# Performance work log

Measured on AMD Instinct MI355X. Metric: run time of the kernel, lower is better.

The kernel has to match this reference:

```python
import jax, jax.numpy as jnp
import numpy as np

D_MODEL = 1024
N_HEAD = 16
D_HEAD = D_MODEL // N_HEAD
D_FF = 4096
EPS = 1e-5


def _layernorm(x, gamma, beta):
    mu = jnp.mean(x, axis=-1, keepdims=True)
    var = jnp.mean(jnp.square(x - mu), axis=-1, keepdims=True)
    return (x - mu) * jax.lax.rsqrt(var + EPS) * gamma + beta


def setup_inputs() -> dict:
    key = jax.random.key(0)
    ks = jax.random.split(key, 16)
    s = 1.0 / np.sqrt(D_MODEL)
    sf = 1.0 / np.sqrt(D_FF)
    return {
        "src": jax.random.normal(ks[0], (8, 1024, D_MODEL), dtype=jnp.float32),
        "Wq": jax.random.uniform(ks[1], (D_MODEL, D_MODEL), jnp.float32, -s, s),
        "bq": jnp.zeros((D_MODEL,), jnp.float32),
        "Wk": jax.random.uniform(ks[2], (D_MODEL, D_MODEL), jnp.float32, -s, s),
        "bk": jnp.zeros((D_MODEL,), jnp.float32),
        "Wv": jax.random.uniform(ks[3], (D_MODEL, D_MODEL), jnp.float32, -s, s),
        "bv": jnp.zeros((D_MODEL,), jnp.float32),
        "Wo": jax.random.uniform(ks[4], (D_MODEL, D_MODEL), jnp.float32, -s, s),
        "bo": jnp.zeros((D_MODEL,), jnp.float32),
        "W1": jax.random.uniform(ks[5], (D_MODEL, D_FF), jnp.float32, -s, s),
        "b1": jnp.zeros((D_FF,), jnp.float32),
        "W2": jax.random.uniform(ks[6], (D_FF, D_MODEL), jnp.float32, -sf, sf),
        "b2": jnp.zeros((D_MODEL,), jnp.float32),
        "g1": jnp.ones((D_MODEL,), jnp.float32),
        "beta1": jnp.zeros((D_MODEL,), jnp.float32),
        "g2": jnp.ones((D_MODEL,), jnp.float32),
        "beta2": jnp.zeros((D_MODEL,), jnp.float32),
    }


def reference(src, Wq, bq, Wk, bk, Wv, bv, Wo, bo, W1, b1, W2, b2, g1, beta1, g2, beta2):
    B, S, _ = src.shape
    x = _layernorm(src, g1, beta1)
    # QKV projections -> [B, H, S, Dh]
    def split_heads(t):
        return t.reshape(B, S, N_HEAD, D_HEAD).transpose(0, 2, 1, 3)
    q = split_heads(x @ Wq + bq)
    k = split_heads(x @ Wk + bk)
    v = split_heads(x @ Wv + bv)
    # SymbolicAttention (canonical graph): softmax(q k^T / sqrt(d_head)) v
    scores = jnp.einsum('bhqd,bhkd->bhqk', q, k) / np.sqrt(D_HEAD).astype(np.float32)
    attn = jax.nn.softmax(scores, axis=-1)
    ctx = jnp.einsum('bhqk,bhkd->bhqd', attn, v)
    ctx = ctx.transpose(0, 2, 1, 3).reshape(B, S, D_MODEL)
    src = src + (ctx @ Wo + bo)  # dropout is identity in eval
    y = _layernorm(src, g2, beta2)
    ffn = jax.nn.relu(y @ W1 + b1) @ W2 + b2
    return src + ffn
```

## Files before the change

### kernel.cpp

```cpp
#include <hip/hip_runtime.h>
#include <stdint.h>

#define D_MODEL 1024
#define N_HEAD  16
#define D_HEAD  64
#define D_FF    4096
#define SEQ     1024
#define BATCH   8
#define M_TOK   (BATCH*SEQ)

typedef __attribute__((ext_vector_type(8))) short bf16x8;
typedef __attribute__((ext_vector_type(4))) float f32x4;

__device__ __forceinline__ float bf2f(unsigned short u) {
    union { unsigned int u; float f; } x; x.u = ((unsigned int)u) << 16; return x.f;
}
__device__ __forceinline__ unsigned short f2bf(float f) {
    union { float f; unsigned int u; } x; x.f = f;
    unsigned int r = x.u + 0x7fffu + ((x.u >> 16) & 1u);
    return (unsigned short)(r >> 16);
}

typedef const __attribute__((address_space(1))) unsigned int* gas_t;
typedef __attribute__((address_space(3))) unsigned int* las_t;
__device__ __forceinline__ void gl_lds16(const unsigned short* g, unsigned short* l) {
    __builtin_amdgcn_global_load_lds((gas_t)g, (las_t)l, 16, 0, 0);
}

__global__ __launch_bounds__(256) void transpose_cvt(
        const float* __restrict__ src, unsigned short* __restrict__ dst,
        int R, int C)
{
    __shared__ float t[32][33];
    const int tx = threadIdx.x & 31, ty = threadIdx.x >> 5;
    const int c0 = blockIdx.x * 32, r0 = blockIdx.y * 32;
    #pragma unroll
    for (int i = 0; i < 32; i += 8)
        t[ty + i][tx] = src[(size_t)(r0 + ty + i) * C + c0 + tx];
    __syncthreads();
    #pragma unroll
    for (int i = 0; i < 32; i += 8)
        dst[(size_t)(c0 + ty + i) * R + r0 + tx] = f2bf(t[tx][ty + i]);
}

__global__ __launch_bounds__(256) void ln_kernel(
        const float* __restrict__ x, const float* __restrict__ g,
        const float* __restrict__ be, unsigned short* __restrict__ out)
{
    const int row = blockIdx.x, tid = threadIdx.x;
    const f32x4 v = *(const f32x4*)(x + (size_t)row * D_MODEL + tid * 4);
    float s  = v[0] + v[1] + v[2] + v[3];
    float ss = v[0]*v[0] + v[1]*v[1] + v[2]*v[2] + v[3]*v[3];
    #pragma unroll
    for (int o = 1; o < 64; o <<= 1) { s += __shfl_xor(s, o); ss += __shfl_xor(ss, o); }
    __shared__ float sa[4], sb[4];
    const int wv = tid >> 6;
    if ((tid & 63) == 0) { sa[wv] = s; sb[wv] = ss; }
    __syncthreads();
    s  = sa[0] + sa[1] + sa[2] + sa[3];
    ss = sb[0] + sb[1] + sb[2] + sb[3];
    const float mu   = s * (1.0f / D_MODEL);
    const float rstd = rsqrtf(ss * (1.0f / D_MODEL) - mu * mu + 1e-5f);
    const f32x4 gv = *(const f32x4*)(g  + tid * 4);
    const f32x4 bv = *(const f32x4*)(be + tid * 4);
    unsigned short w[4];
    #pragma unroll
    for (int j = 0; j < 4; j++) w[j] = f2bf((v[j] - mu) * rstd * gv[j] + bv[j]);
    *(uint2*)(out + (size_t)row * D_MODEL + tid * 4) = *(uint2*)w;
}

template<int MODE>
__global__ __launch_bounds__(256) void gemm_bf16_tn(
        const unsigned short* __restrict__ A,
        const unsigned short* __restrict__ BT,
        const float* __restrict__ bias,
        const float* __restrict__ bias2,
        const float* __restrict__ bias3,
        const float* __restrict__ resid,
        void* __restrict__ Cout,
        int M, int N, int K)
{
    constexpr bool SWAP = (MODE != 3);
    __shared__ unsigned short As[128 * 64];
    __shared__ unsigned short Bs[128 * 64];

    const int tid  = threadIdx.x;
    const int wave = tid >> 6, lane = tid & 63;
    const int quad = lane >> 4, l16 = lane & 15;

    int m0, n0;
    if (MODE == 2) {
        const int G = gridDim.x;
        const int f = blockIdx.x + G * blockIdx.y;
        m0 = ((f & 7) + 8 * ((f >> 3) / G)) * 128;
        n0 = ((f >> 3) % G) * 128;
    } else {
        m0 = blockIdx.y * 128;
        n0 = blockIdx.x * 128;
    }
    const int wm = (wave >> 1) * 64, wn = (wave & 1) * 64;

    const int st_row = wave * 8 + ((tid >> 3) & 7);
    const int st_g   = (tid & 7) ^ ((tid >> 3) & 7);
    const unsigned short* gA = A  + (size_t)(m0 + st_row) * K + st_g * 8;
    const unsigned short* gB = BT + (size_t)(n0 + st_row) * K + st_g * 8;
    unsigned short* lA = As + wave * 512;
    unsigned short* lB = Bs + wave * 512;
    const int rx = l16 & 7;

    f32x4 acc[4][4] = {};

    for (int k0 = 0; k0 < K; k0 += 64) {
        __syncthreads();
        #pragma unroll
        for (int j = 0; j < 4; j++) {
            gl_lds16(gA + (size_t)j * 32 * K + k0, lA + j * 2048);
            gl_lds16(gB + (size_t)j * 32 * K + k0, lB + j * 2048);
        }
        __syncthreads();

        #pragma unroll
        for (int h = 0; h < 2; h++) {
            bf16x8 af[4], bfr[4];
            #pragma unroll
            for (int mi = 0; mi < 4; mi++)
                af[mi] = *(const bf16x8*)(As + (wm + mi * 16 + l16) * 64
                                          + ((h * 4 + quad) ^ rx) * 8);
            #pragma unroll
            for (int ni = 0; ni < 4; ni++)
                bfr[ni] = *(const bf16x8*)(Bs + (wn + ni * 16 + l16) * 64
                                           + ((h * 4 + quad) ^ rx) * 8);
            #pragma unroll
            for (int mi = 0; mi < 4; mi++)
                #pragma unroll
                for (int ni = 0; ni < 4; ni++)
                    acc[mi][ni] = SWAP
                        ? __builtin_amdgcn_mfma_f32_16x16x32_bf16(
                              bfr[ni], af[mi], acc[mi][ni], 0, 0, 0)
                        : __builtin_amdgcn_mfma_f32_16x16x32_bf16(
                              af[mi], bfr[ni], acc[mi][ni], 0, 0, 0);
        }
    }

    if (SWAP) {
        #pragma unroll
        for (int mi = 0; mi < 4; mi++) {
            const int row = m0 + wm + mi * 16 + l16;
            #pragma unroll
            for (int ni = 0; ni < 4; ni++) {
                const int col = n0 + wn + ni * 16 + quad * 4;
                const f32x4 bs4 = *(const f32x4*)(bias + col);
                if (MODE == 1) {
                    unsigned short w[4];
                    #pragma unroll
                    for (int r = 0; r < 4; r++)
                        w[r] = f2bf(fmaxf(acc[mi][ni][r] + bs4[r], 0.0f));
                    *(uint2*)((unsigned short*)Cout + (size_t)row * N + col)
                        = *(uint2*)w;
                } else {
                    const f32x4 rv = *(const f32x4*)(resid + (size_t)row * N + col);
                    f32x4 o;
                    #pragma unroll
                    for (int r = 0; r < 4; r++)
                        o[r] = acc[mi][ni][r] + bs4[r] + rv[r];
                    *(f32x4*)((float*)Cout + (size_t)row * N + col) = o;
                }
            }
        }
    } else {
        #pragma unroll
        for (int mi = 0; mi < 4; mi++) {
            const int row_b = m0 + wm + mi * 16 + quad * 4;
            #pragma unroll
            for (int ni = 0; ni < 4; ni++) {
                const int col = n0 + wn + ni * 16 + l16;
                if (col < 2048) {
                    const float sc  = (col < 1024) ? 0.125f : 1.0f;
                    const float bsv = (col < 1024) ? bias[col] : bias2[col - 1024];
                    unsigned short* dst = (unsigned short*)Cout
                        + (size_t)(col >> 10) * M_TOK * 1024;
                    #pragma unroll
                    for (int r = 0; r < 4; r++)
                        dst[(size_t)(row_b + r) * 1024 + (col & 1023)] =
                            f2bf((acc[mi][ni][r] + bsv) * sc);
                } else {
                    const int cc = col - 2048;
                    const float bsv = bias3[cc];
                    const int bb = row_b >> 10, s = row_b & 1023;
                    const int h = cc >> 6, dd = cc & 63;
                    unsigned short w[4];
                    #pragma unroll
                    for (int r = 0; r < 4; r++)
                        w[r] = f2bf(acc[mi][ni][r] + bsv);
                    *(uint2*)((unsigned short*)Cout + (size_t)2 * M_TOK * 1024
                              + ((size_t)((bb * 16 + h) * 64 + dd)) * 1024 + s)
                        = *(uint2*)w;
                }
            }
        }
    }
}

#define ASTR 72
__global__ __launch_bounds__(256) void attn_mfma(
        const unsigned short* __restrict__ Q,
        const unsigned short* __restrict__ K,
        const unsigned short* __restrict__ VT,
        unsigned short* __restrict__ CTX)
{
    __shared__ unsigned short Ks[64 * ASTR];
    __shared__ unsigned short Vs[64 * ASTR];
    __shared__ unsigned short Ps[128 * ASTR];

    const int tid  = threadIdx.x;
    const int wave = tid >> 6, lane = tid & 63;
    const int quad = lane >> 4, l16 = lane & 15;
    const int bh = blockIdx.y;
    const int q0 = blockIdx.x * 128;
    const size_t baseQ = (size_t)(bh >> 4) * SEQ * D_MODEL + (size_t)(bh & 15) * D_HEAD;
    const size_t baseV = (size_t)bh * D_HEAD * SEQ;
    const int strip = wave * 32;

    bf16x8 qf[2][2];
    #pragma unroll
    for (int mt = 0; mt < 2; mt++)
        #pragma unroll
        for (int h = 0; h < 2; h++)
            qf[mt][h] = *(const bf16x8*)(Q + baseQ
                        + (size_t)(q0 + strip + mt * 16 + l16) * D_MODEL
                        + h * 32 + quad * 8);

    f32x4 of[2][4] = {};
    float l_p[2][4] = {};

    for (int c = 0; c < SEQ / 64; c++) {
        const int k0 = c * 64;
        __syncthreads();
        #pragma unroll
        for (int u = tid; u < 512; u += 256) {
            const int r = u >> 3, g = (u & 7) * 8;
            *(uint4*)(Ks + r * ASTR + g) =
                *(const uint4*)(K + baseQ + (size_t)(k0 + r) * D_MODEL + g);
            *(uint4*)(Vs + r * ASTR + g) =
                *(const uint4*)(VT + baseV + (size_t)r * SEQ + k0 + g);
        }
        __syncthreads();

        bf16x8 kf[4][2];
        #pragma unroll
        for (int kt = 0; kt < 4; kt++)
            #pragma unroll
            for (int h = 0; h < 2; h++)
                kf[kt][h] = *(const bf16x8*)(Ks + (kt * 16 + l16) * ASTR + h * 32 + quad * 8);

        #pragma unroll
        for (int mt = 0; mt < 2; mt++) {
            f32x4 s[4] = {};
            #pragma unroll
            for (int h = 0; h < 2; h++)
                #pragma unroll
                for (int kt = 0; kt < 4; kt++)
                    s[kt] = __builtin_amdgcn_mfma_f32_16x16x32_bf16(
                            qf[mt][h], kf[kt][h], s[kt], 0, 0, 0);
            #pragma unroll
            for (int kt = 0; kt < 4; kt++)
                #pragma unroll
                for (int r = 0; r < 4; r++) {
                    const float p = __expf(s[kt][r]);
                    l_p[mt][r] += p;
                    Ps[(strip + mt * 16 + quad * 4 + r) * ASTR + kt * 16 + l16] = f2bf(p);
                }
        }

        bf16x8 pf[2][2];
        #pragma unroll
        for (int mt = 0; mt < 2; mt++)
            #pragma unroll
            for (int h = 0; h < 2; h++)
                pf[mt][h] = *(const bf16x8*)(Ps + (strip + mt * 16 + l16) * ASTR
                                             + h * 32 + quad * 8);
        #pragma unroll
        for (int nt = 0; nt < 4; nt++) {
            bf16x8 vf[2];
            #pragma unroll
            for (int h = 0; h < 2; h++)
                vf[h] = *(const bf16x8*)(Vs + (nt * 16 + l16) * ASTR + h * 32 + quad * 8);
            #pragma unroll
            for (int mt = 0; mt < 2; mt++)
                #pragma unroll
                for (int h = 0; h < 2; h++)
                    of[mt][nt] = __builtin_amdgcn_mfma_f32_16x16x32_bf16(
                            pf[mt][h], vf[h], of[mt][nt], 0, 0, 0);
        }
    }

    #pragma unroll
    for (int mt = 0; mt < 2; mt++) {
        float inv[4];
        #pragma unroll
        for (int r = 0; r < 4; r++) {
            float l = l_p[mt][r];
            #pragma unroll
            for (int o = 1; o < 16; o <<= 1) l += __shfl_xor(l, o);
            inv[r] = 1.0f / l;
        }
        #pragma unroll
        for (int nt = 0; nt < 4; nt++)
            #pragma unroll
            for (int r = 0; r < 4; r++)
                CTX[baseQ + (size_t)(q0 + strip + mt * 16 + quad * 4 + r) * D_MODEL
                    + nt * 16 + l16] = f2bf(of[mt][nt][r] * inv[r]);
    }
}

extern "C" void kernel_launch(void* const* d_in, const int* in_sizes, int n_in,
                              void* d_out, int out_size, void* d_ws, size_t ws_size,
                              hipStream_t stream)
{
    (void)in_sizes; (void)n_in; (void)out_size; (void)ws_size;
    const float* src = (const float*)d_in[0];
    const float* Wq  = (const float*)d_in[1];
    const float* bq  = (const float*)d_in[2];
    const float* Wk  = (const float*)d_in[3];
    const float* bk  = (const float*)d_in[4];
    const float* Wv  = (const float*)d_in[5];
    const float* bv  = (const float*)d_in[6];
    const float* Wo  = (const float*)d_in[7];
    const float* bo  = (const float*)d_in[8];
    const float* W1  = (const float*)d_in[9];
    const float* b1  = (const float*)d_in[10];
    const float* W2  = (const float*)d_in[11];
    const float* b2  = (const float*)d_in[12];
    const float* g1  = (const float*)d_in[13];
    const float* be1 = (const float*)d_in[14];
    const float* g2  = (const float*)d_in[15];
    const float* be2 = (const float*)d_in[16];
    float* out = (float*)d_out;

    unsigned short* wqkvT = (unsigned short*)d_ws;
    unsigned short* woT = wqkvT + (size_t)3 * 1024 * 1024;
    unsigned short* w1T = woT + 1024 * 1024;
    unsigned short* w2T = w1T + (size_t)4096 * 1024;
    unsigned short* xn  = w2T + (size_t)1024 * 4096;
    unsigned short* q   = xn  + (size_t)M_TOK * D_MODEL;
    unsigned short* k   = q   + (size_t)M_TOK * D_MODEL;
    unsigned short* vT  = k   + (size_t)M_TOK * D_MODEL;
    unsigned short* ctx = vT  + (size_t)M_TOK * D_MODEL;
    unsigned short* hid = ctx + (size_t)M_TOK * D_MODEL;

    const dim3 blk(256);

    transpose_cvt<<<dim3(32, 32),  blk, 0, stream>>>(Wq, wqkvT,                 1024, 1024);
    transpose_cvt<<<dim3(32, 32),  blk, 0, stream>>>(Wk, wqkvT + 1024 * 1024,   1024, 1024);
    transpose_cvt<<<dim3(32, 32),  blk, 0, stream>>>(Wv, wqkvT + 2 * 1024 * 1024, 1024, 1024);
    transpose_cvt<<<dim3(32, 32),  blk, 0, stream>>>(Wo, woT, 1024, 1024);
    transpose_cvt<<<dim3(128, 32), blk, 0, stream>>>(W1, w1T, 1024, 4096);
    transpose_cvt<<<dim3(32, 128), blk, 0, stream>>>(W2, w2T, 4096, 1024);

    ln_kernel<<<M_TOK, blk, 0, stream>>>(src, g1, be1, xn);

    gemm_bf16_tn<3><<<dim3(24, 64), blk, 0, stream>>>(
        xn, wqkvT, bq, bk, bv, nullptr, q, M_TOK, 3072, D_MODEL);

    attn_mfma<<<dim3(SEQ / 128, BATCH * N_HEAD), blk, 0, stream>>>(q, k, vT, ctx);

    gemm_bf16_tn<2><<<dim3(8, 64), blk, 0, stream>>>(
        ctx, woT, bo, nullptr, nullptr, src, out, M_TOK, D_MODEL, D_MODEL);

    ln_kernel<<<M_TOK, blk, 0, stream>>>(out, g2, be2, xn);

    gemm_bf16_tn<1><<<dim3(32, 64), blk, 0, stream>>>(
        xn, w1T, b1, nullptr, nullptr, nullptr, hid, M_TOK, D_FF, D_MODEL);

    gemm_bf16_tn<2><<<dim3(8, 64), blk, 0, stream>>>(
        hid, w2T, b2, nullptr, nullptr, out, out, M_TOK, D_MODEL, D_FF);
}
```

Before: 501.0 us.

## Switch GEMMs to 32x32x16 MFMA and split QKV projection into QK and V launches

All GEMM variants now use 32x32x16 bf16 MFMA with 2x2 accumulator tiles per wave instead of 16x16x32 with 4x4 tiles. This halves the LDS fragment loads per MFMA and gives wider contiguous epilogue writes. The fused QKV projection is split in two: Q/K go through a row-major mode with vectorized stores, and V goes through a separate transposed-store launch. That removes the per-element strided scalar stores for Q and K, at the cost of one extra kernel launch.

After: 536.8 us. 7.2% more time.

```diff
diff --git a/kernel.cpp b/kernel.cpp
--- a/kernel.cpp
+++ b/kernel.cpp
@@ -9,8 +9,9 @@
 #define BATCH   8
 #define M_TOK   (BATCH*SEQ)
 
-typedef __attribute__((ext_vector_type(8))) short bf16x8;
-typedef __attribute__((ext_vector_type(4))) float f32x4;
+typedef __attribute__((ext_vector_type(8)))  short bf16x8;
+typedef __attribute__((ext_vector_type(4)))  float f32x4;
+typedef __attribute__((ext_vector_type(16))) float f32x16;
 
 __device__ __forceinline__ float bf2f(unsigned short u) {
     union { unsigned int u; float f; } x; x.u = ((unsigned int)u) << 16; return x.f;
@@ -75,7 +76,6 @@
         const unsigned short* __restrict__ BT,
         const float* __restrict__ bias,
         const float* __restrict__ bias2,
-        const float* __restrict__ bias3,
         const float* __restrict__ resid,
         void* __restrict__ Cout,
         int M, int N, int K)
@@ -86,7 +86,7 @@
 
     const int tid  = threadIdx.x;
     const int wave = tid >> 6, lane = tid & 63;
-    const int quad = lane >> 4, l16 = lane & 15;
+    const int l32 = lane & 31, khalf = lane >> 5;
 
     int m0, n0;
     if (MODE == 2) {
@@ -106,9 +106,9 @@
     const unsigned short* gB = BT + (size_t)(n0 + st_row) * K + st_g * 8;
     unsigned short* lA = As + wave * 512;
     unsigned short* lB = Bs + wave * 512;
-    const int rx = l16 & 7;
-
-    f32x4 acc[4][4] = {};
+    const int rx = l32 & 7;
+
+    f32x16 acc[2][2] = {};
 
     for (int k0 = 0; k0 < K; k0 += 64) {
         __syncthreads();
@@ -120,79 +120,84 @@
         __syncthreads();
 
         #pragma unroll
-        for (int h = 0; h < 2; h++) {
-            bf16x8 af[4], bfr[4];
-            #pragma unroll
-            for (int mi = 0; mi < 4; mi++)
-                af[mi] = *(const bf16x8*)(As + (wm + mi * 16 + l16) * 64
-                                          + ((h * 4 + quad) ^ rx) * 8);
-            #pragma unroll
-            for (int ni = 0; ni < 4; ni++)
-                bfr[ni] = *(const bf16x8*)(Bs + (wn + ni * 16 + l16) * 64
-                                           + ((h * 4 + quad) ^ rx) * 8);
-            #pragma unroll
-            for (int mi = 0; mi < 4; mi++)
-                #pragma unroll
-                for (int ni = 0; ni < 4; ni++)
+        for (int s = 0; s < 4; s++) {
+            const int slot = ((s * 2 + khalf) ^ rx) * 8;
+            bf16x8 af[2], bfr[2];
+            #pragma unroll
+            for (int mi = 0; mi < 2; mi++)
+                af[mi] = *(const bf16x8*)(As + (wm + mi * 32 + l32) * 64 + slot);
+            #pragma unroll
+            for (int ni = 0; ni < 2; ni++)
+                bfr[ni] = *(const bf16x8*)(Bs + (wn + ni * 32 + l32) * 64 + slot);
+            #pragma unroll
+            for (int mi = 0; mi < 2; mi++)
+                #pragma unroll
+                for (int ni = 0; ni < 2; ni++)
                     acc[mi][ni] = SWAP
-                        ? __builtin_amdgcn_mfma_f32_16x16x32_bf16(
+                        ? __builtin_amdgcn_mfma_f32_32x32x16_bf16(
                               bfr[ni], af[mi], acc[mi][ni], 0, 0, 0)
-                        : __builtin_amdgcn_mfma_f32_16x16x32_bf16(
+                        : __builtin_amdgcn_mfma_f32_32x32x16_bf16(
                               af[mi], bfr[ni], acc[mi][ni], 0, 0, 0);
         }
     }
 
     if (SWAP) {
         #pragma unroll
-        for (int mi = 0; mi < 4; mi++) {
-            const int row = m0 + wm + mi * 16 + l16;
-            #pragma unroll
-            for (int ni = 0; ni < 4; ni++) {
-                const int col = n0 + wn + ni * 16 + quad * 4;
-                const f32x4 bs4 = *(const f32x4*)(bias + col);
-                if (MODE == 1) {
+        for (int mi = 0; mi < 2; mi++) {
+            const int row = m0 + wm + mi * 32 + l32;
+            #pragma unroll
+            for (int ni = 0; ni < 2; ni++) {
+                #pragma unroll
+                for (int g = 0; g < 4; g++) {
+                    const int col = n0 + wn + ni * 32 + 8 * g + 4 * khalf;
+                    if (MODE == 1) {
+                        const f32x4 b4 = *(const f32x4*)(bias + col);
+                        unsigned short w[4];
+                        #pragma unroll
+                        for (int r = 0; r < 4; r++)
+                            w[r] = f2bf(fmaxf(acc[mi][ni][4 * g + r] + b4[r], 0.0f));
+                        *(uint2*)((unsigned short*)Cout + (size_t)row * N + col)
+                            = *(uint2*)w;
+                    } else if (MODE == 2) {
+                        const f32x4 b4 = *(const f32x4*)(bias + col);
+                        const f32x4 rv = *(const f32x4*)(resid + (size_t)row * N + col);
+                        f32x4 o;
+                        #pragma unroll
+                        for (int r = 0; r < 4; r++)
+                            o[r] = acc[mi][ni][4 * g + r] + b4[r] + rv[r];
+                        *(f32x4*)((float*)Cout + (size_t)row * N + col) = o;
+                    } else {
+                        const float sc = (col < 1024) ? 0.125f : 1.0f;
+                        const f32x4 b4 = *(const f32x4*)(
+                            ((col < 1024) ? bias : bias2) + (col & 1023));
+                        unsigned short w[4];
+                        #pragma unroll
+                        for (int r = 0; r < 4; r++)
+                            w[r] = f2bf((acc[mi][ni][4 * g + r] + b4[r]) * sc);
+                        *(uint2*)((unsigned short*)Cout
+                                  + (size_t)(col >> 10) * M_TOK * 1024
+                                  + (size_t)row * 1024 + (col & 1023)) = *(uint2*)w;
+                    }
+                }
+            }
+        }
+    } else {
+        #pragma unroll
+        for (int mi = 0; mi < 2; mi++) {
+            #pragma unroll
+            for (int ni = 0; ni < 2; ni++) {
+                const int col = n0 + wn + ni * 32 + l32;
+                const float bsv = bias[col];
+                const int h = col >> 6, dd = col & 63;
+                #pragma unroll
+                for (int g = 0; g < 4; g++) {
+                    const int rowb = m0 + wm + mi * 32 + 8 * g + 4 * khalf;
+                    const int bb = rowb >> 10, s = rowb & 1023;
                     unsigned short w[4];
                     #pragma unroll
                     for (int r = 0; r < 4; r++)
-                        w[r] = f2bf(fmaxf(acc[mi][ni][r] + bs4[r], 0.0f));
-                    *(uint2*)((unsigned short*)Cout + (size_t)row * N + col)
-                        = *(uint2*)w;
-                } else {
-                    const f32x4 rv = *(const f32x4*)(resid + (size_t)row * N + col);
-                    f32x4 o;
-                    #pragma unroll
-                    for (int r = 0; r < 4; r++)
-                        o[r] = acc[mi][ni][r] + bs4[r] + rv[r];
-                    *(f32x4*)((float*)Cout + (size_t)row * N + col) = o;
-                }
-            }
-        }
-    } else {
-        #pragma unroll
-        for (int mi = 0; mi < 4; mi++) {
-            const int row_b = m0 + wm + mi * 16 + quad * 4;
-            #pragma unroll
-            for (int ni = 0; ni < 4; ni++) {
-                const int col = n0 + wn + ni * 16 + l16;
-                if (col < 2048) {
-                    const float sc  = (col < 1024) ? 0.125f : 1.0f;
-                    const float bsv = (col < 1024) ? bias[col] : bias2[col - 1024];
-                    unsigned short* dst = (unsigned short*)Cout
-                        + (size_t)(col >> 10) * M_TOK * 1024;
-                    #pragma unroll
-                    for (int r = 0; r < 4; r++)
-                        dst[(size_t)(row_b + r) * 1024 + (col & 1023)] =
-                            f2bf((acc[mi][ni][r] + bsv) * sc);
-                } else {
-                    const int cc = col - 2048;
-                    const float bsv = bias3[cc];
-                    const int bb = row_b >> 10, s = row_b & 1023;
-                    const int h = cc >> 6, dd = cc & 63;
-                    unsigned short w[4];
-                    #pragma unroll
-                    for (int r = 0; r < 4; r++)
-                        w[r] = f2bf(acc[mi][ni][r] + bsv);
-                    *(uint2*)((unsigned short*)Cout + (size_t)2 * M_TOK * 1024
+                        w[r] = f2bf(acc[mi][ni][4 * g + r] + bsv);
+                    *(uint2*)((unsigned short*)Cout
                               + ((size_t)((bb * 16 + h) * 64 + dd)) * 1024 + s)
                         = *(uint2*)w;
                 }
@@ -337,8 +342,9 @@
     const float* be2 = (const float*)d_in[16];
     float* out = (float*)d_out;
 
-    unsigned short* wqkvT = (unsigned short*)d_ws;
-    unsigned short* woT = wqkvT + (size_t)3 * 1024 * 1024;
+    unsigned short* wqkT = (unsigned short*)d_ws;
+    unsigned short* wvT = wqkT + (size_t)2 * 1024 * 1024;
+    unsigned short* woT = wvT + 1024 * 1024;
     unsigned short* w1T = woT + 1024 * 1024;
     unsigned short* w2T = w1T + (size_t)4096 * 1024;
     unsigned short* xn  = w2T + (size_t)1024 * 4096;
@@ -350,28 +356,30 @@
 
     const dim3 blk(256);
 
-    transpose_cvt<<<dim3(32, 32),  blk, 0, stream>>>(Wq, wqkvT,                 1024, 1024);
-    transpose_cvt<<<dim3(32, 32),  blk, 0, stream>>>(Wk, wqkvT + 1024 * 1024,   1024, 1024);
-    transpose_cvt<<<dim3(32, 32),  blk, 0, stream>>>(Wv, wqkvT + 2 * 1024 * 1024, 1024, 1024);
+    transpose_cvt<<<dim3(32, 32),  blk, 0, stream>>>(Wq, wqkT,               1024, 1024);
+    transpose_cvt<<<dim3(32, 32),  blk, 0, stream>>>(Wk, wqkT + 1024 * 1024, 1024, 1024);
+    transpose_cvt<<<dim3(32, 32),  blk, 0, stream>>>(Wv, wvT, 1024, 1024);
     transpose_cvt<<<dim3(32, 32),  blk, 0, stream>>>(Wo, woT, 1024, 1024);
     transpose_cvt<<<dim3(128, 32), blk, 0, stream>>>(W1, w1T, 1024, 4096);
     transpose_cvt<<<dim3(32, 128), blk, 0, stream>>>(W2, w2T, 4096, 1024);
 
     ln_kernel<<<M_TOK, blk, 0, stream>>>(src, g1, be1, xn);
 
-    gemm_bf16_tn<3><<<dim3(24, 64), blk, 0, stream>>>(
-        xn, wqkvT, bq, bk, bv, nullptr, q, M_TOK, 3072, D_MODEL);
+    gemm_bf16_tn<4><<<dim3(16, 64), blk, 0, stream>>>(
+        xn, wqkT, bq, bk, nullptr, q, M_TOK, 2048, D_MODEL);
+    gemm_bf16_tn<3><<<dim3(8, 64), blk, 0, stream>>>(
+        xn, wvT, bv, nullptr, nullptr, vT, M_TOK, D_MODEL, D_MODEL);
 
     attn_mfma<<<dim3(SEQ / 128, BATCH * N_HEAD), blk, 0, stream>>>(q, k, vT, ctx);
 
     gemm_bf16_tn<2><<<dim3(8, 64), blk, 0, stream>>>(
-        ctx, woT, bo, nullptr, nullptr, src, out, M_TOK, D_MODEL, D_MODEL);
+        ctx, woT, bo, nullptr, src, out, M_TOK, D_MODEL, D_MODEL);
 
     ln_kernel<<<M_TOK, blk, 0, stream>>>(out, g2, be2, xn);
 
     gemm_bf16_tn<1><<<dim3(32, 64), blk, 0, stream>>>(
-        xn, w1T, b1, nullptr, nullptr, nullptr, hid, M_TOK, D_FF, D_MODEL);
+        xn, w1T, b1, nullptr, nullptr, hid, M_TOK, D_FF, D_MODEL);
 
     gemm_bf16_tn<2><<<dim3(8, 64), blk, 0, stream>>>(
-        hid, w2T, b2, nullptr, nullptr, out, out, M_TOK, D_MODEL, D_FF);
-}
+        hid, w2T, b2, nullptr, out, out, M_TOK, D_MODEL, D_FF);
+}
```
